# Optimization experiments

Measured on AMD Instinct MI355X. Metric: run time of the kernel, lower is better.

## Reference

```python
import jax, jax.numpy as jnp
import numpy as np

N = 50000   # nodes
C = 128     # in == hidden == out channels (required by residual add)
E = 500000  # edges (before self-loops)
H = 64      # hidden width of pos_nn / attn_nn


def setup_inputs() -> dict:
    key = jax.random.key(0)
    ks = jax.random.split(key, 20)
    s = lambda fan_in: 1.0 / np.sqrt(fan_in)
    d = {}
    d["x"] = jax.random.normal(ks[0], (N, C), jnp.float32)
    d["pos"] = jax.random.uniform(ks[1], (N, 3), jnp.float32)
    d["edge_index"] = jax.random.randint(ks[2], (2, E), 0, N, dtype=jnp.int32)
    # lin_in / lin_out (with bias)
    d["W_in"] = jax.random.normal(ks[3], (C, C), jnp.float32) * s(C)
    d["b_in"] = jnp.zeros((C,), jnp.float32)
    d["W_out"] = jax.random.normal(ks[4], (C, C), jnp.float32) * s(C)
    d["b_out"] = jnp.zeros((C,), jnp.float32)
    # PointTransformerConv internal linears (bias=False in PyG)
    d["W_lin"] = jax.random.normal(ks[5], (C, C), jnp.float32) * s(C)
    d["W_src"] = jax.random.normal(ks[6], (C, C), jnp.float32) * s(C)
    d["W_dst"] = jax.random.normal(ks[7], (C, C), jnp.float32) * s(C)
    # pos_nn: Lin(3,64) -> ReLU -> Lin(64,C)
    d["Wp1"] = jax.random.normal(ks[8], (3, H), jnp.float32) * s(3)
    d["bp1"] = jnp.zeros((H,), jnp.float32)
    d["Wp2"] = jax.random.normal(ks[9], (H, C), jnp.float32) * s(H)
    d["bp2"] = jnp.zeros((C,), jnp.float32)
    # attn_nn: Lin(C,64) -> ReLU -> Lin(64,C)
    d["Wa1"] = jax.random.normal(ks[10], (C, H), jnp.float32) * s(C)
    d["ba1"] = jnp.zeros((H,), jnp.float32)
    d["Wa2"] = jax.random.normal(ks[11], (H, C), jnp.float32) * s(H)
    d["ba2"] = jnp.zeros((C,), jnp.float32)
    return d


def reference(x, pos, edge_index, W_in, b_in, W_out, b_out, W_lin, W_src, W_dst,
              Wp1, bp1, Wp2, bp2, Wa1, ba1, Wa2, ba2):
    n = x.shape[0]
    x_skip = x
    h = jax.nn.relu(x @ W_in + b_in)                      # lin_in + relu, [N,C]
    # PointTransformerConv with add_self_loops=True
    loop = jnp.arange(n, dtype=edge_index.dtype)
    src = jnp.concatenate([edge_index[0], loop])          # j (source)
    dst = jnp.concatenate([edge_index[1], loop])          # i (target)
    a_src = h @ W_src                                      # lin_src(x), [N,C]
    a_dst = h @ W_dst                                      # lin_dst(x), [N,C]
    v = h @ W_lin                                          # lin(x),     [N,C]
    rel = pos[dst] - pos[src]                              # pos_i - pos_j, [Et,3]
    delta = jax.nn.relu(rel @ Wp1 + bp1) @ Wp2 + bp2       # pos_nn, [Et,C]
    alpha = a_dst[dst] - a_src[src] + delta                # alpha_i - alpha_j + delta
    alpha = jax.nn.relu(alpha @ Wa1 + ba1) @ Wa2 + ba2     # attn_nn, [Et,C]
    # per-destination, per-channel softmax over edges
    amax = jax.ops.segment_max(alpha, dst, num_segments=n)
    amax = jnp.where(jnp.isfinite(amax), amax, 0.0)
    ex = jnp.exp(alpha - amax[dst])
    den = jax.ops.segment_sum(ex, dst, num_segments=n) + 1e-16
    w = ex / den[dst]
    out = jax.ops.segment_sum(w * (v[src] + delta), dst, num_segments=n)  # [N,C]
    out = jax.nn.relu(out @ W_out + b_out)                 # lin_out + relu
    return out + x_skip
```

## Files before the change

### kernel.cpp

```cpp
#include <hip/hip_runtime.h>

typedef _Float16 h2_t __attribute__((ext_vector_type(2)));
typedef _Float16 f16x4v __attribute__((ext_vector_type(4)));
typedef _Float16 f16x8 __attribute__((ext_vector_type(8)));
typedef float f32x4 __attribute__((ext_vector_type(4)));

struct F8pair { f16x4v lo, hi; };
static __device__ __forceinline__ f16x8 ldfrag(const _Float16* p) {
    F8pair r;
    r.lo = *(const f16x4v*)p;
    r.hi = *(const f16x4v*)(p + 4);
    return __builtin_bit_cast(f16x8, r);
}

static __device__ __forceinline__ unsigned int pkrtz(float a, float b) {
    return __builtin_bit_cast(unsigned int, __builtin_amdgcn_cvt_pkrtz(a, b));
}

static __device__ __forceinline__ float h2lo(unsigned int w) {
    h2_t h = __builtin_bit_cast(h2_t, w);
    return (float)h.x;
}
static __device__ __forceinline__ float h2hi(unsigned int w) {
    h2_t h = __builtin_bit_cast(h2_t, w);
    return (float)h.y;
}

__global__ void k_pre(const float* __restrict__ W_src, const float* __restrict__ W_dst,
                      const float* __restrict__ Wa1, const float* __restrict__ ba1,
                      const float* __restrict__ Wp2, const float* __restrict__ bp2,
                      const float* __restrict__ Wa2,
                      float* __restrict__ PsW, float* __restrict__ PdW,
                      float* __restrict__ bias2, _Float16* __restrict__ Wcat)
{
    int idx = blockIdx.x * 256 + threadIdx.x;
    if (idx < 8192) {
        int k = idx >> 6, l = idx & 63;
        float a = 0.f;
        for (int c = 0; c < 128; ++c) a = fmaf(W_src[k*128+c], Wa1[c*64+l], a);
        PsW[idx] = a;
    } else if (idx < 16384) {
        int j = idx - 8192; int k = j >> 6, l = j & 63;
        float a = 0.f;
        for (int c = 0; c < 128; ++c) a = fmaf(W_dst[k*128+c], Wa1[c*64+l], a);
        PdW[j] = a;
    } else if (idx < 16448) {
        int l = idx - 16384;
        float a = ba1[l];
        for (int c = 0; c < 128; ++c) a = fmaf(bp2[c], Wa1[c*64+l], a);
        bias2[l] = a;
    } else if (idx < 16448 + 320*68) {
        int j = idx - 16448;
        int row = j / 68, k = j % 68;
        float val = 0.f;
        if (k < 64) {
            if (row < 64) {
                int Q = 2 * (row & 31) + (row >> 5);
                float a = 0.f;
                for (int c = 0; c < 128; ++c) a = fmaf(Wp2[k*128+c], Wa1[c*64+Q], a);
                val = a;
            } else if (row < 192) {
                int cpos = row - 64;
                int P = 2 * (cpos & 63) + (cpos >> 6);
                val = Wp2[k*128 + P];
            } else {
                int cpos = row - 192;
                int P = 2 * (cpos & 63) + (cpos >> 6);
                int Qk = 2 * (k & 31) + (k >> 5);
                val = Wa2[Qk*128 + P];
            }
        }
        Wcat[j] = (_Float16)val;
    }
}

__global__ void k_zero(int* __restrict__ p, int n) {
    int i = blockIdx.x * 256 + threadIdx.x;
    if (i < n) p[i] = 0;
}

__global__ void k_count(const int* __restrict__ ei, int E, int N, int* __restrict__ cnt) {
    int i = blockIdx.x * 256 + threadIdx.x;
    int T = E + N;
    if (i >= T) return;
    int dst = (i < E) ? ei[E + i] : (i - E);
    atomicAdd(&cnt[dst], 1);
}

__global__ void k_pos4(const float* __restrict__ pos, float4* __restrict__ pos4, int N) {
    int i = blockIdx.x * 256 + threadIdx.x;
    if (i < N) pos4[i] = make_float4(pos[3*i], pos[3*i+1], pos[3*i+2], 0.f);
}

__global__ __launch_bounds__(1024) void k_scan1(int* __restrict__ cnt, int* __restrict__ bsum, int N) {
    __shared__ int sc[1024];
    int t = threadIdx.x;
    int i = blockIdx.x * 1024 + t;
    int val = (i < N) ? cnt[i] : 0;
    sc[t] = val;
    __syncthreads();
    for (int off = 1; off < 1024; off <<= 1) {
        int tmp = (t >= off) ? sc[t - off] : 0;
        __syncthreads();
        sc[t] += tmp;
        __syncthreads();
    }
    int incl = sc[t];
    if (i < N) cnt[i] = incl - val;
    if (t == 1023) bsum[blockIdx.x] = incl;
}

__global__ void k_scan2(int* __restrict__ bsum, int* __restrict__ offs, int nb, int N) {
    if (threadIdx.x == 0 && blockIdx.x == 0) {
        int run = 0;
        for (int i = 0; i < nb; ++i) { int tv = bsum[i]; bsum[i] = run; run += tv; }
        offs[N] = run;
    }
}

__global__ void k_scan3(int* __restrict__ offs, const int* __restrict__ bsum,
                        int* __restrict__ cursor, int N) {
    int i = blockIdx.x * 256 + threadIdx.x;
    if (i < N) {
        int o = offs[i] + bsum[i >> 10];
        offs[i] = o;
        cursor[i] = o;
    }
}

__global__ void k_scatter(const int* __restrict__ ei, int E, int N,
                          int* __restrict__ cursor, int* __restrict__ srcs) {
    int i = blockIdx.x * 256 + threadIdx.x;
    int T = E + N;
    if (i >= T) return;
    int s_, d_;
    if (i < E) { s_ = ei[i]; d_ = ei[E + i]; }
    else       { s_ = i - E; d_ = i - E; }
    int p = atomicAdd(&cursor[d_], 1);
    srcs[p] = s_;
}

__global__ __launch_bounds__(256) void k_node(
    const float* __restrict__ x, const float* __restrict__ W_in, const float* __restrict__ b_in,
    const float* __restrict__ W_lin, const float* __restrict__ PsW, const float* __restrict__ PdW,
    const float* __restrict__ bp2,
    unsigned int* __restrict__ vpk, unsigned int* __restrict__ pspk,
    unsigned int* __restrict__ pdpk, int N)
{
    __shared__ float xsT[128][20];
    __shared__ float hsT[128][20];
    int t = threadIdx.x;
    int r0 = blockIdx.x * 16;

    for (int idx = t; idx < 16 * 128; idx += 256) {
        int r = idx >> 7, k = idx & 127;
        int row = r0 + r;
        xsT[k][r] = (row < N) ? x[row * 128 + k] : 0.f;
    }
    __syncthreads();

    int c = t & 127, rg = t >> 7;
    float acc[8];
    {
        float b = b_in[c];
        #pragma unroll
        for (int j = 0; j < 8; ++j) acc[j] = b;
        for (int k = 0; k < 128; ++k) {
            float w = W_in[k * 128 + c];
            const float4 xa = *(const float4*)&xsT[k][rg * 8];
            const float4 xb = *(const float4*)&xsT[k][rg * 8 + 4];
            acc[0] = fmaf(xa.x, w, acc[0]); acc[1] = fmaf(xa.y, w, acc[1]);
            acc[2] = fmaf(xa.z, w, acc[2]); acc[3] = fmaf(xa.w, w, acc[3]);
            acc[4] = fmaf(xb.x, w, acc[4]); acc[5] = fmaf(xb.y, w, acc[5]);
            acc[6] = fmaf(xb.z, w, acc[6]); acc[7] = fmaf(xb.w, w, acc[7]);
        }
        #pragma unroll
        for (int j = 0; j < 8; ++j) hsT[c][rg * 8 + j] = fmaxf(acc[j], 0.f);
    }
    __syncthreads();
    {
        #pragma unroll
        for (int j = 0; j < 8; ++j) acc[j] = 0.f;
        for (int k = 0; k < 128; ++k) {
            float w = W_lin[k * 128 + c];
            const float4 ha = *(const float4*)&hsT[k][rg * 8];
            const float4 hb = *(const float4*)&hsT[k][rg * 8 + 4];
            acc[0] = fmaf(ha.x, w, acc[0]); acc[1] = fmaf(ha.y, w, acc[1]);
            acc[2] = fmaf(ha.z, w, acc[2]); acc[3] = fmaf(ha.w, w, acc[3]);
            acc[4] = fmaf(hb.x, w, acc[4]); acc[5] = fmaf(hb.y, w, acc[5]);
            acc[6] = fmaf(hb.z, w, acc[6]); acc[7] = fmaf(hb.w, w, acc[7]);
        }
        float bpA = bp2[c], bpB = bp2[c | 1];
        #pragma unroll
        for (int j = 0; j < 8; ++j) {
            float partner = __shfl_xor(acc[j], 1);
            int row = r0 + rg * 8 + j;
            if (((c & 1) == 0) && row < N)
                vpk[(size_t)row * 64 + (c >> 1)] = pkrtz(acc[j] + bpA, partner + bpB);
        }
    }
    {
        int c2 = t & 63, g = t >> 6;
        float as[4], ad[4];
        #pragma unroll
        for (int j = 0; j < 4; ++j) { as[j] = 0.f; ad[j] = 0.f; }
        for (int k = 0; k < 128; ++k) {
            float wsv = PsW[k * 64 + c2];
            float wdv = PdW[k * 64 + c2];
            const float4 h4 = *(const float4*)&hsT[k][g * 4];
            as[0] = fmaf(h4.x, wsv, as[0]); as[1] = fmaf(h4.y, wsv, as[1]);
            as[2] = fmaf(h4.z, wsv, as[2]); as[3] = fmaf(h4.w, wsv, as[3]);
            ad[0] = fmaf(h4.x, wdv, ad[0]); ad[1] = fmaf(h4.y, wdv, ad[1]);
            ad[2] = fmaf(h4.z, wdv, ad[2]); ad[3] = fmaf(h4.w, wdv, ad[3]);
        }
        #pragma unroll
        for (int j = 0; j < 4; ++j) {
            float pa = __shfl_xor(as[j], 1);
            float pb = __shfl_xor(ad[j], 1);
            int row = r0 + g * 4 + j;
            if (((c2 & 1) == 0) && row < N) {
                pspk[(size_t)row * 32 + (c2 >> 1)] = pkrtz(as[j], pa);
                pdpk[(size_t)row * 32 + (c2 >> 1)] = pkrtz(ad[j], pb);
            }
        }
    }
}

__global__ __launch_bounds__(512, 2) void k_edge(
    const unsigned int* __restrict__ vpk, const unsigned int* __restrict__ pspk,
    const unsigned int* __restrict__ pdpk,
    const float4* __restrict__ pos4, const int* __restrict__ srcs,
    const int* __restrict__ offs, const _Float16* __restrict__ Wcat,
    const float* __restrict__ Wp1, const float* __restrict__ bp1,
    const float* __restrict__ bias2,
    float* __restrict__ out, int N, int nWavesTot)
{
    __shared__ _Float16 WL[320 * 68];
    __shared__ _Float16 PH[8][16 * 68];
    int tid = threadIdx.x;
    {
        const unsigned int* g = (const unsigned int*)Wcat;
        unsigned int* s = (unsigned int*)WL;
        for (int i = tid; i < 320 * 68 / 2; i += 512) s[i] = g[i];
    }
    __syncthreads();

    int wid = tid >> 6, lane = tid & 63;
    int l15 = lane & 15, akg = lane >> 4;
    _Float16* ph  = PH[wid];
    _Float16* ahv = ph;

    float wp10 = Wp1[lane], wp11 = Wp1[64 + lane], wp12 = Wp1[128 + lane], bp1l = bp1[lane];
    float bias2_r[4];
    #pragma unroll
    for (int nt = 0; nt < 4; ++nt)
        bias2_r[nt] = bias2[2 * ((nt & 1) * 16 + l15) + (nt >> 1)];

    int gw = blockIdx.x * 8 + wid;
    for (int node = gw; node < N; node += nWavesTot) {
        int beg = offs[node], end = offs[node + 1];
        float4 pi = pos4[node];
        unsigned int pdw0 = pdpk[(size_t)node * 32 + l15];
        unsigned int pdw1 = pdpk[(size_t)node * 32 + 16 + l15];
        float base4[4];
        #pragma unroll
        for (int nt = 0; nt < 4; ++nt) {
            unsigned int wd = (nt & 1) ? pdw1 : pdw0;
            base4[nt] = ((nt >> 1) ? h2hi(wd) : h2lo(wd)) + bias2_r[nt];
        }

        float rn[8], rd[8];
        #pragma unroll
        for (int nt = 0; nt < 8; ++nt) { rn[nt] = 0.f; rd[nt] = 0.f; }

        for (int e0 = beg; e0 < end; e0 += 16) {
            int ei_ = e0 + l15;
            int eim = (ei_ < end) ? ei_ : (end - 1);
            int s16 = srcs[eim];
            float4 pj = pos4[s16];
            if (akg == 0) {
                uint2 rr;
                rr.x = pkrtz(pi.x - pj.x, pi.y - pj.y);
                rr.y = pkrtz(pi.z - pj.z, 0.f);
                *(uint2*)&ph[l15 * 68 + 64] = rr;
            }
            #pragma unroll
            for (int ee = 0; ee < 16; ++ee) {
                uint2 rr = *(const uint2*)&ph[ee * 68 + 64];
                float rx = h2lo(rr.x), ry = h2hi(rr.x), rz = h2lo(rr.y);
                float phv = fmaxf(fmaf(rx, wp10, fmaf(ry, wp11, fmaf(rz, wp12, bp1l))), 0.f);
                ph[ee * 68 + lane] = (_Float16)phv;
            }

            f16x8 A0 = ldfrag(&ph[l15 * 68 + akg * 8]);
            f16x8 A1 = ldfrag(&ph[l15 * 68 + 32 + akg * 8]);

            int se[4];
            #pragma unroll
            for (int j = 0; j < 4; ++j) se[j] = __shfl(s16, akg * 4 + j);

            {
                unsigned int psw0[4], psw1[4];
                #pragma unroll
                for (int j = 0; j < 4; ++j) {
                    psw0[j] = pspk[(size_t)se[j] * 32 + l15];
                    psw1[j] = pspk[(size_t)se[j] * 32 + 16 + l15];
                }
                #pragma unroll
                for (int nt = 0; nt < 4; ++nt) {
                    const _Float16* br = &WL[(nt * 16 + l15) * 68];
                    f16x8 B0 = ldfrag(br + akg * 8);
                    f16x8 B1 = ldfrag(br + 32 + akg * 8);
                    f32x4 a = {0.f, 0.f, 0.f, 0.f};
                    a = __builtin_amdgcn_mfma_f32_16x16x32_f16(A0, B0, a, 0, 0, 0);
                    a = __builtin_amdgcn_mfma_f32_16x16x32_f16(A1, B1, a, 0, 0, 0);
                    #pragma unroll
                    for (int j = 0; j < 4; ++j) {
                        unsigned int ws = (nt & 1) ? psw1[j] : psw0[j];
                        float psv = (nt >> 1) ? h2hi(ws) : h2lo(ws);
                        float ahf = fmaxf(a[j] + base4[nt] - psv, 0.f);
                        ahv[(akg * 4 + j) * 68 + nt * 16 + l15] = (_Float16)ahf;
                    }
                }
            }

            f16x8 C0 = ldfrag(&ahv[l15 * 68 + akg * 8]);
            f16x8 C1 = ldfrag(&ahv[l15 * 68 + 32 + akg * 8]);

            #pragma unroll
            for (int hf = 0; hf < 2; ++hf) {
                unsigned int wvA[4], wvB[4];
                #pragma unroll
                for (int j = 0; j < 4; ++j) {
                    wvA[j] = vpk[(size_t)se[j] * 64 + hf * 32 + l15];
                    wvB[j] = vpk[(size_t)se[j] * 64 + hf * 32 + 16 + l15];
                }
                #pragma unroll
                for (int q = 0; q < 4; ++q) {
                    int nt = (q & 1) + hf * 2 + (q >> 1) * 4;
                    const _Float16* br2 = &WL[(64 + nt * 16 + l15) * 68];
                    f16x8 B20 = ldfrag(br2 + akg * 8);
                    f16x8 B21 = ldfrag(br2 + 32 + akg * 8);
                    f32x4 a2 = {0.f, 0.f, 0.f, 0.f};
                    a2 = __builtin_amdgcn_mfma_f32_16x16x32_f16(A0, B20, a2, 0, 0, 0);
                    a2 = __builtin_amdgcn_mfma_f32_16x16x32_f16(A1, B21, a2, 0, 0, 0);
                    const _Float16* br3 = &WL[(192 + nt * 16 + l15) * 68];
                    f16x8 B30 = ldfrag(br3 + akg * 8);
                    f16x8 B31 = ldfrag(br3 + 32 + akg * 8);
                    f32x4 a3 = {0.f, 0.f, 0.f, 0.f};
                    a3 = __builtin_amdgcn_mfma_f32_16x16x32_f16(C0, B30, a3, 0, 0, 0);
                    a3 = __builtin_amdgcn_mfma_f32_16x16x32_f16(C1, B31, a3, 0, 0, 0);
                    #pragma unroll
                    for (int j = 0; j < 4; ++j) {
                        bool vj = (e0 + akg * 4 + j) < end;
                        unsigned int wv = (q & 1) ? wvB[j] : wvA[j];
                        float vv = (q >> 1) ? h2hi(wv) : h2lo(wv);
                        float alpha = vj ? a3[j] : -1e30f;
                        float wexp = __expf(fminf(alpha, 60.f));
                        float u = vv + a2[j];
                        rd[nt] += wexp;
                        rn[nt] = fmaf(wexp, u, rn[nt]);
                    }
                }
            }
        }

        #pragma unroll
        for (int nt = 0; nt < 8; ++nt) {
            rn[nt] += __shfl_xor(rn[nt], 16);
            rn[nt] += __shfl_xor(rn[nt], 32);
            rd[nt] += __shfl_xor(rd[nt], 16);
            rd[nt] += __shfl_xor(rd[nt], 32);
        }
        if (akg == 0) {
            #pragma unroll
            for (int nt2 = 0; nt2 < 4; ++nt2) {
                float2 o;
                o.x = rn[nt2]     / (rd[nt2]     + 1e-16f);
                o.y = rn[nt2 + 4] / (rd[nt2 + 4] + 1e-16f);
                ((float2*)out)[(size_t)node * 64 + nt2 * 16 + l15] = o;
            }
        }
    }
}

__global__ __launch_bounds__(256) void k_out(
    const float* __restrict__ x, const float* __restrict__ W_out, const float* __restrict__ b_out,
    float* __restrict__ out, int N)
{
    __shared__ float csT[128][20];
    int t = threadIdx.x;
    int r0 = blockIdx.x * 16;

    for (int idx = t; idx < 16 * 128; idx += 256) {
        int r = idx >> 7, k = idx & 127;
        int row = r0 + r;
        csT[k][r] = (row < N) ? out[row * 128 + k] : 0.f;
    }
    __syncthreads();

    int c = t & 127, rg = t >> 7;
    float acc[8];
    float b = b_out[c];
    #pragma unroll
    for (int j = 0; j < 8; ++j) acc[j] = b;
    for (int k = 0; k < 128; ++k) {
        float w = W_out[k * 128 + c];
        const float4 ca = *(const float4*)&csT[k][rg * 8];
        const float4 cb = *(const float4*)&csT[k][rg * 8 + 4];
        acc[0] = fmaf(ca.x, w, acc[0]); acc[1] = fmaf(ca.y, w, acc[1]);
        acc[2] = fmaf(ca.z, w, acc[2]); acc[3] = fmaf(ca.w, w, acc[3]);
        acc[4] = fmaf(cb.x, w, acc[4]); acc[5] = fmaf(cb.y, w, acc[5]);
        acc[6] = fmaf(cb.z, w, acc[6]); acc[7] = fmaf(cb.w, w, acc[7]);
    }
    #pragma unroll
    for (int j = 0; j < 8; ++j) {
        int row = r0 + rg * 8 + j;
        if (row < N) out[row * 128 + c] = fmaxf(acc[j], 0.f) + x[row * 128 + c];
    }
}

extern "C" void kernel_launch(void* const* d_in, const int* in_sizes, int n_in,
                              void* d_out, int out_size, void* d_ws, size_t ws_size,
                              hipStream_t stream)
{
    const float* x     = (const float*)d_in[0];
    const float* pos   = (const float*)d_in[1];
    const int*   ei    = (const int*)d_in[2];
    const float* W_in  = (const float*)d_in[3];
    const float* b_in  = (const float*)d_in[4];
    const float* W_out = (const float*)d_in[5];
    const float* b_out = (const float*)d_in[6];
    const float* W_lin = (const float*)d_in[7];
    const float* W_src = (const float*)d_in[8];
    const float* W_dst = (const float*)d_in[9];
    const float* Wp1   = (const float*)d_in[10];
    const float* bp1   = (const float*)d_in[11];
    const float* Wp2   = (const float*)d_in[12];
    const float* bp2   = (const float*)d_in[13];
    const float* Wa1   = (const float*)d_in[14];
    const float* ba1   = (const float*)d_in[15];
    const float* Wa2   = (const float*)d_in[16];
    const float* ba2   = (const float*)d_in[17];
    (void)ba2;

    int N = in_sizes[0] / 128;
    int E = in_sizes[2] / 2;
    int T = E + N;
    float* out = (float*)d_out;

    char* w = (char*)d_ws;
    auto alloc = [&](size_t bytes) -> char* {
        char* p = w;
        w += (bytes + 255) & ~(size_t)255;
        return p;
    };
    unsigned int* vpk  = (unsigned int*)alloc((size_t)N * 64 * 4);
    unsigned int* pspk = (unsigned int*)alloc((size_t)N * 32 * 4);
    unsigned int* pdpk = (unsigned int*)alloc((size_t)N * 32 * 4);
    float4* pos4 = (float4*)alloc((size_t)N * 16);
    float* PsW   = (float*)alloc(8192 * 4);
    float* PdW   = (float*)alloc(8192 * 4);
    float* bias2 = (float*)alloc(64 * 4);
    _Float16* Wcat = (_Float16*)alloc(320 * 68 * 2);
    int*   offs  = (int*)alloc((size_t)(N + 1) * 4);
    int*   cursor= (int*)alloc((size_t)N * 4);
    int*   bsum  = (int*)alloc(256 * 4);
    int*   srcs  = (int*)alloc((size_t)T * 4);

    k_pre<<<dim3((16448 + 320*68 + 255) / 256), dim3(256), 0, stream>>>(
        W_src, W_dst, Wa1, ba1, Wp2, bp2, Wa2, PsW, PdW, bias2, Wcat);
    k_zero<<<dim3((N + 1 + 255) / 256), dim3(256), 0, stream>>>(offs, N + 1);
    k_count<<<dim3((T + 255) / 256), dim3(256), 0, stream>>>(ei, E, N, offs);
    k_pos4<<<dim3((N + 255) / 256), dim3(256), 0, stream>>>(pos, pos4, N);
    int nb = (N + 1023) / 1024;
    k_scan1<<<dim3(nb), dim3(1024), 0, stream>>>(offs, bsum, N);
    k_scan2<<<dim3(1), dim3(64), 0, stream>>>(bsum, offs, nb, N);
    k_scan3<<<dim3((N + 255) / 256), dim3(256), 0, stream>>>(offs, bsum, cursor, N);
    k_scatter<<<dim3((T + 255) / 256), dim3(256), 0, stream>>>(ei, E, N, cursor, srcs);
    k_node<<<dim3((N + 15) / 16), dim3(256), 0, stream>>>(x, W_in, b_in, W_lin, PsW, PdW, bp2,
                                                          vpk, pspk, pdpk, N);
    int nWavesTot = 8192;
    k_edge<<<dim3(1024), dim3(512), 0, stream>>>(vpk, pspk, pdpk, pos4, srcs, offs, Wcat,
                                                 Wp1, bp1, bias2,
                                                 out, N, nWavesTot);
    k_out<<<dim3((N + 15) / 16), dim3(256), 0, stream>>>(x, W_out, b_out, out, N);
}
```

Before: 378.2 us.

## Move node and output dense layers to fp16 MFMA with persistent waves

Replaces the scalar fp32 FMA node kernel (lin_in, lin, and the fused src/dst attention projections) and the output linear kernel with MFMA 16x16x32 fp16 versions. Each kernel is persistent, loads pre-transposed, padded fp16 weights into shared memory once per block, and loops each wave over 16-row tiles. The weight transposition and fp16 conversion move into the precompute kernel. The inputs x and the aggregated features are rounded to fp16, and lin_in's output is also rounded to fp16 between layers, which lowers precision. Each node block now holds about 100KB of shared memory, which limits occupancy.

```diff
diff --git a/kernel.cpp b/kernel.cpp
--- a/kernel.cpp
+++ b/kernel.cpp
@@ -26,31 +26,31 @@
     return (float)h.y;
 }
 
+static __device__ __forceinline__ f16x8 mkfrag(const float* p) {
+    float4 a = ((const float4*)p)[0];
+    float4 b = ((const float4*)p)[1];
+    uint4 u;
+    u.x = pkrtz(a.x, a.y); u.y = pkrtz(a.z, a.w);
+    u.z = pkrtz(b.x, b.y); u.w = pkrtz(b.z, b.w);
+    return __builtin_bit_cast(f16x8, u);
+}
+
 __global__ void k_pre(const float* __restrict__ W_src, const float* __restrict__ W_dst,
                       const float* __restrict__ Wa1, const float* __restrict__ ba1,
                       const float* __restrict__ Wp2, const float* __restrict__ bp2,
-                      const float* __restrict__ Wa2,
-                      float* __restrict__ PsW, float* __restrict__ PdW,
-                      float* __restrict__ bias2, _Float16* __restrict__ Wcat)
+                      const float* __restrict__ Wa2, const float* __restrict__ W_in,
+                      const float* __restrict__ W_lin, const float* __restrict__ W_out,
+                      float* __restrict__ bias2, _Float16* __restrict__ Wcat,
+                      _Float16* __restrict__ Wnode, _Float16* __restrict__ WoutT)
 {
     int idx = blockIdx.x * 256 + threadIdx.x;
-    if (idx < 8192) {
-        int k = idx >> 6, l = idx & 63;
-        float a = 0.f;
-        for (int c = 0; c < 128; ++c) a = fmaf(W_src[k*128+c], Wa1[c*64+l], a);
-        PsW[idx] = a;
-    } else if (idx < 16384) {
-        int j = idx - 8192; int k = j >> 6, l = j & 63;
-        float a = 0.f;
-        for (int c = 0; c < 128; ++c) a = fmaf(W_dst[k*128+c], Wa1[c*64+l], a);
-        PdW[j] = a;
-    } else if (idx < 16448) {
-        int l = idx - 16384;
+    if (idx < 64) {
+        int l = idx;
         float a = ba1[l];
         for (int c = 0; c < 128; ++c) a = fmaf(bp2[c], Wa1[c*64+l], a);
         bias2[l] = a;
-    } else if (idx < 16448 + 320*68) {
-        int j = idx - 16448;
+    } else if (idx < 64 + 21760) {
+        int j = idx - 64;
         int row = j / 68, k = j % 68;
         float val = 0.f;
         if (k < 64) {
@@ -71,6 +71,30 @@
             }
         }
         Wcat[j] = (_Float16)val;
+    } else if (idx < 21824 + 16896) {
+        int j = idx - 21824;
+        int c = j / 132, k = j % 132;
+        Wnode[j] = (_Float16)((k < 128) ? W_in[k*128+c] : 0.f);
+    } else if (idx < 38720 + 16896) {
+        int j = idx - 38720;
+        int c = j / 132, k = j % 132;
+        Wnode[16896 + j] = (_Float16)((k < 128) ? W_lin[k*128+c] : 0.f);
+    } else if (idx < 55616 + 16896) {
+        int j = idx - 55616;
+        int c = j / 132, k = j % 132;
+        float val = 0.f;
+        if (k < 128) {
+            if (c < 64) {
+                for (int q = 0; q < 128; ++q) val = fmaf(W_src[k*128+q], Wa1[q*64+c], val);
+            } else {
+                for (int q = 0; q < 128; ++q) val = fmaf(W_dst[k*128+q], Wa1[q*64+(c-64)], val);
+            }
+        }
+        Wnode[33792 + j] = (_Float16)val;
+    } else if (idx < 72512 + 16896) {
+        int j = idx - 72512;
+        int c = j / 132, k = j % 132;
+        WoutT[j] = (_Float16)((k < 128) ? W_out[k*128+c] : 0.f);
     }
 }
 
@@ -140,87 +164,90 @@
     srcs[p] = s_;
 }
 
-__global__ __launch_bounds__(256) void k_node(
-    const float* __restrict__ x, const float* __restrict__ W_in, const float* __restrict__ b_in,
-    const float* __restrict__ W_lin, const float* __restrict__ PsW, const float* __restrict__ PdW,
-    const float* __restrict__ bp2,
+__global__ __launch_bounds__(512) void k_node2(
+    const float* __restrict__ x, const float* __restrict__ b_in,
+    const float* __restrict__ bp2, const _Float16* __restrict__ Wnode,
     unsigned int* __restrict__ vpk, unsigned int* __restrict__ pspk,
-    unsigned int* __restrict__ pdpk, int N)
+    unsigned int* __restrict__ pdpk, int N, int nTiles, int nWavesTot)
 {
-    __shared__ float xsT[128][20];
-    __shared__ float hsT[128][20];
-    int t = threadIdx.x;
-    int r0 = blockIdx.x * 16;
-
-    for (int idx = t; idx < 16 * 128; idx += 256) {
-        int r = idx >> 7, k = idx & 127;
-        int row = r0 + r;
-        xsT[k][r] = (row < N) ? x[row * 128 + k] : 0.f;
+    __shared__ _Float16 WB[3 * 16896];
+    __shared__ _Float16 HT[8][16 * 132];
+    int tid = threadIdx.x;
+    {
+        const unsigned int* g = (const unsigned int*)Wnode;
+        unsigned int* s = (unsigned int*)WB;
+        for (int i = tid; i < 3 * 16896 / 2; i += 512) s[i] = g[i];
     }
     __syncthreads();
 
-    int c = t & 127, rg = t >> 7;
-    float acc[8];
-    {
-        float b = b_in[c];
-        #pragma unroll
-        for (int j = 0; j < 8; ++j) acc[j] = b;
-        for (int k = 0; k < 128; ++k) {
-            float w = W_in[k * 128 + c];
-            const float4 xa = *(const float4*)&xsT[k][rg * 8];
-            const float4 xb = *(const float4*)&xsT[k][rg * 8 + 4];
-            acc[0] = fmaf(xa.x, w, acc[0]); acc[1] = fmaf(xa.y, w, acc[1]);
-            acc[2] = fmaf(xa.z, w, acc[2]); acc[3] = fmaf(xa.w, w, acc[3]);
-            acc[4] = fmaf(xb.x, w, acc[4]); acc[5] = fmaf(xb.y, w, acc[5]);
-            acc[6] = fmaf(xb.z, w, acc[6]); acc[7] = fmaf(xb.w, w, acc[7]);
-        }
-        #pragma unroll
-        for (int j = 0; j < 8; ++j) hsT[c][rg * 8 + j] = fmaxf(acc[j], 0.f);
-    }
-    __syncthreads();
-    {
-        #pragma unroll
-        for (int j = 0; j < 8; ++j) acc[j] = 0.f;
-        for (int k = 0; k < 128; ++k) {
-            float w = W_lin[k * 128 + c];
-            const float4 ha = *(const float4*)&hsT[k][rg * 8];
-            const float4 hb = *(const float4*)&hsT[k][rg * 8 + 4];
-            acc[0] = fmaf(ha.x, w, acc[0]); acc[1] = fmaf(ha.y, w, acc[1]);
-            acc[2] = fmaf(ha.z, w, acc[2]); acc[3] = fmaf(ha.w, w, acc[3]);
-            acc[4] = fmaf(hb.x, w, acc[4]); acc[5] = fmaf(hb.y, w, acc[5]);
-            acc[6] = fmaf(hb.z, w, acc[6]); acc[7] = fmaf(hb.w, w, acc[7]);
-        }
-        float bpA = bp2[c], bpB = bp2[c | 1];
-        #pragma unroll
-        for (int j = 0; j < 8; ++j) {
-            float partner = __shfl_xor(acc[j], 1);
-            int row = r0 + rg * 8 + j;
-            if (((c & 1) == 0) && row < N)
-                vpk[(size_t)row * 64 + (c >> 1)] = pkrtz(acc[j] + bpA, partner + bpB);
-        }
-    }
-    {
-        int c2 = t & 63, g = t >> 6;
-        float as[4], ad[4];
-        #pragma unroll
-        for (int j = 0; j < 4; ++j) { as[j] = 0.f; ad[j] = 0.f; }
-        for (int k = 0; k < 128; ++k) {
-            float wsv = PsW[k * 64 + c2];
-            float wdv = PdW[k * 64 + c2];
-            const float4 h4 = *(const float4*)&hsT[k][g * 4];
-            as[0] = fmaf(h4.x, wsv, as[0]); as[1] = fmaf(h4.y, wsv, as[1]);
-            as[2] = fmaf(h4.z, wsv, as[2]); as[3] = fmaf(h4.w, wsv, as[3]);
-            ad[0] = fmaf(h4.x, wdv, ad[0]); ad[1] = fmaf(h4.y, wdv, ad[1]);
-            ad[2] = fmaf(h4.z, wdv, ad[2]); ad[3] = fmaf(h4.w, wdv, ad[3]);
-        }
-        #pragma unroll
-        for (int j = 0; j < 4; ++j) {
-            float pa = __shfl_xor(as[j], 1);
-            float pb = __shfl_xor(ad[j], 1);
-            int row = r0 + g * 4 + j;
-            if (((c2 & 1) == 0) && row < N) {
-                pspk[(size_t)row * 32 + (c2 >> 1)] = pkrtz(as[j], pa);
-                pdpk[(size_t)row * 32 + (c2 >> 1)] = pkrtz(ad[j], pb);
+    int wid = tid >> 6, lane = tid & 63;
+    int l15 = lane & 15, akg = lane >> 4;
+    _Float16* ht = HT[wid];
+
+    int gw = blockIdx.x * 8 + wid;
+    for (int t = gw; t < nTiles; t += nWavesTot) {
+        int row0 = t * 16;
+        int rowa = row0 + l15; if (rowa > N - 1) rowa = N - 1;
+
+        f16x8 A[4];
+        #pragma unroll
+        for (int f = 0; f < 4; ++f)
+            A[f] = mkfrag(&x[(size_t)rowa * 128 + f * 32 + akg * 8]);
+
+        #pragma unroll
+        for (int ct = 0; ct < 8; ++ct) {
+            const _Float16* bb = &WB[(ct * 16 + l15) * 132];
+            f32x4 d = {0.f, 0.f, 0.f, 0.f};
+            #pragma unroll
+            for (int f = 0; f < 4; ++f)
+                d = __builtin_amdgcn_mfma_f32_16x16x32_f16(A[f], ldfrag(bb + f * 32 + akg * 8), d, 0, 0, 0);
+            float bin = b_in[ct * 16 + l15];
+            #pragma unroll
+            for (int j = 0; j < 4; ++j)
+                ht[(akg * 4 + j) * 132 + ct * 16 + l15] = (_Float16)fmaxf(d[j] + bin, 0.f);
+        }
+
+        f16x8 H[4];
+        #pragma unroll
+        for (int f = 0; f < 4; ++f)
+            H[f] = ldfrag(&ht[l15 * 132 + f * 32 + akg * 8]);
+
+        #pragma unroll
+        for (int ct = 0; ct < 8; ++ct) {
+            const _Float16* bb = &WB[16896 + (ct * 16 + l15) * 132];
+            f32x4 d = {0.f, 0.f, 0.f, 0.f};
+            #pragma unroll
+            for (int f = 0; f < 4; ++f)
+                d = __builtin_amdgcn_mfma_f32_16x16x32_f16(H[f], ldfrag(bb + f * 32 + akg * 8), d, 0, 0, 0);
+            float bp = bp2[ct * 16 + l15];
+            #pragma unroll
+            for (int j = 0; j < 4; ++j) {
+                float val = d[j] + bp;
+                float partner = __shfl_xor(val, 1);
+                int row = row0 + akg * 4 + j;
+                if (((l15 & 1) == 0) && row < N)
+                    vpk[(size_t)row * 64 + ct * 8 + (l15 >> 1)] = pkrtz(val, partner);
+            }
+        }
+
+        #pragma unroll
+        for (int ct = 0; ct < 8; ++ct) {
+            const _Float16* bb = &WB[33792 + (ct * 16 + l15) * 132];
+            f32x4 d = {0.f, 0.f, 0.f, 0.f};
+            #pragma unroll
+            for (int f = 0; f < 4; ++f)
+                d = __builtin_amdgcn_mfma_f32_16x16x32_f16(H[f], ldfrag(bb + f * 32 + akg * 8), d, 0, 0, 0);
+            #pragma unroll
+            for (int j = 0; j < 4; ++j) {
+                float val = d[j];
+                float partner = __shfl_xor(val, 1);
+                int row = row0 + akg * 4 + j;
+                if (((l15 & 1) == 0) && row < N) {
+                    if (ct < 4)
+                        pspk[(size_t)row * 32 + ct * 8 + (l15 >> 1)] = pkrtz(val, partner);
+                    else
+                        pdpk[(size_t)row * 32 + (ct - 4) * 8 + (l15 >> 1)] = pkrtz(val, partner);
+                }
             }
         }
     }
@@ -384,39 +411,50 @@
     }
 }
 
-__global__ __launch_bounds__(256) void k_out(
-    const float* __restrict__ x, const float* __restrict__ W_out, const float* __restrict__ b_out,
-    float* __restrict__ out, int N)
+__global__ __launch_bounds__(256) void k_out2(
+    const float* __restrict__ x, const float* __restrict__ b_out,
+    const _Float16* __restrict__ WoutT, float* __restrict__ out,
+    int N, int nTiles, int nWavesTot)
 {
-    __shared__ float csT[128][20];
-    int t = threadIdx.x;
-    int r0 = blockIdx.x * 16;
-
-    for (int idx = t; idx < 16 * 128; idx += 256) {
-        int r = idx >> 7, k = idx & 127;
-        int row = r0 + r;
-        csT[k][r] = (row < N) ? out[row * 128 + k] : 0.f;
+    __shared__ _Float16 WB[16896];
+    int tid = threadIdx.x;
+    {
+        const unsigned int* g = (const unsigned int*)WoutT;
+        unsigned int* s = (unsigned int*)WB;
+        for (int i = tid; i < 16896 / 2; i += 256) s[i] = g[i];
     }
     __syncthreads();
 
-    int c = t & 127, rg = t >> 7;
-    float acc[8];
-    float b = b_out[c];
-    #pragma unroll
-    for (int j = 0; j < 8; ++j) acc[j] = b;
-    for (int k = 0; k < 128; ++k) {
-        float w = W_out[k * 128 + c];
-        const float4 ca = *(const float4*)&csT[k][rg * 8];
-        const float4 cb = *(const float4*)&csT[k][rg * 8 + 4];
-        acc[0] = fmaf(ca.x, w, acc[0]); acc[1] = fmaf(ca.y, w, acc[1]);
-        acc[2] = fmaf(ca.z, w, acc[2]); acc[3] = fmaf(ca.w, w, acc[3]);
-        acc[4] = fmaf(cb.x, w, acc[4]); acc[5] = fmaf(cb.y, w, acc[5]);
-        acc[6] = fmaf(cb.z, w, acc[6]); acc[7] = fmaf(cb.w, w, acc[7]);
-    }
-    #pragma unroll
-    for (int j = 0; j < 8; ++j) {
-        int row = r0 + rg * 8 + j;
-        if (row < N) out[row * 128 + c] = fmaxf(acc[j], 0.f) + x[row * 128 + c];
+    int wid = tid >> 6, lane = tid & 63;
+    int l15 = lane & 15, akg = lane >> 4;
+
+    int gw = blockIdx.x * 4 + wid;
+    for (int t = gw; t < nTiles; t += nWavesTot) {
+        int row0 = t * 16;
+        int rowa = row0 + l15; if (rowa > N - 1) rowa = N - 1;
+
+        f16x8 A[4];
+        #pragma unroll
+        for (int f = 0; f < 4; ++f)
+            A[f] = mkfrag(&out[(size_t)rowa * 128 + f * 32 + akg * 8]);
+
+        #pragma unroll
+        for (int ct = 0; ct < 8; ++ct) {
+            const _Float16* bb = &WB[(ct * 16 + l15) * 132];
+            f32x4 d = {0.f, 0.f, 0.f, 0.f};
+            #pragma unroll
+            for (int f = 0; f < 4; ++f)
+                d = __builtin_amdgcn_mfma_f32_16x16x32_f16(A[f], ldfrag(bb + f * 32 + akg * 8), d, 0, 0, 0);
+            float bo = b_out[ct * 16 + l15];
+            #pragma unroll
+            for (int j = 0; j < 4; ++j) {
+                int row = row0 + akg * 4 + j;
+                if (row < N) {
+                    int c = ct * 16 + l15;
+                    out[(size_t)row * 128 + c] = fmaxf(d[j] + bo, 0.f) + x[(size_t)row * 128 + c];
+                }
+            }
+        }
     }
 }
 
@@ -447,6 +485,7 @@
     int N = in_sizes[0] / 128;
     int E = in_sizes[2] / 2;
     int T = E + N;
+    int nTiles = (N + 15) / 16;
     float* out = (float*)d_out;
 
     char* w = (char*)d_ws;
@@ -459,17 +498,18 @@
     unsigned int* pspk = (unsigned int*)alloc((size_t)N * 32 * 4);
     unsigned int* pdpk = (unsigned int*)alloc((size_t)N * 32 * 4);
     float4* pos4 = (float4*)alloc((size_t)N * 16);
-    float* PsW   = (float*)alloc(8192 * 4);
-    float* PdW   = (float*)alloc(8192 * 4);
     float* bias2 = (float*)alloc(64 * 4);
-    _Float16* Wcat = (_Float16*)alloc(320 * 68 * 2);
+    _Float16* Wcat  = (_Float16*)alloc(21760 * 2);
+    _Float16* Wnode = (_Float16*)alloc(3 * 16896 * 2);
+    _Float16* WoutT = (_Float16*)alloc(16896 * 2);
     int*   offs  = (int*)alloc((size_t)(N + 1) * 4);
     int*   cursor= (int*)alloc((size_t)N * 4);
     int*   bsum  = (int*)alloc(256 * 4);
     int*   srcs  = (int*)alloc((size_t)T * 4);
 
-    k_pre<<<dim3((16448 + 320*68 + 255) / 256), dim3(256), 0, stream>>>(
-        W_src, W_dst, Wa1, ba1, Wp2, bp2, Wa2, PsW, PdW, bias2, Wcat);
+    k_pre<<<dim3((89408 + 255) / 256), dim3(256), 0, stream>>>(
+        W_src, W_dst, Wa1, ba1, Wp2, bp2, Wa2, W_in, W_lin, W_out,
+        bias2, Wcat, Wnode, WoutT);
     k_zero<<<dim3((N + 1 + 255) / 256), dim3(256), 0, stream>>>(offs, N + 1);
     k_count<<<dim3((T + 255) / 256), dim3(256), 0, stream>>>(ei, E, N, offs);
     k_pos4<<<dim3((N + 255) / 256), dim3(256), 0, stream>>>(pos, pos4, N);
@@ -478,11 +518,16 @@
     k_scan2<<<dim3(1), dim3(64), 0, stream>>>(bsum, offs, nb, N);
     k_scan3<<<dim3((N + 255) / 256), dim3(256), 0, stream>>>(offs, bsum, cursor, N);
     k_scatter<<<dim3((T + 255) / 256), dim3(256), 0, stream>>>(ei, E, N, cursor, srcs);
-    k_node<<<dim3((N + 15) / 16), dim3(256), 0, stream>>>(x, W_in, b_in, W_lin, PsW, PdW, bp2,
-                                                          vpk, pspk, pdpk, N);
+
+    int nodeBlocks = 192;
+    k_node2<<<dim3(nodeBlocks), dim3(512), 0, stream>>>(x, b_in, bp2, Wnode,
+                                                        vpk, pspk, pdpk, N, nTiles,
+                                                        nodeBlocks * 8);
     int nWavesTot = 8192;
     k_edge<<<dim3(1024), dim3(512), 0, stream>>>(vpk, pspk, pdpk, pos4, srcs, offs, Wcat,
                                                  Wp1, bp1, bias2,
                                                  out, N, nWavesTot);
-    k_out<<<dim3((N + 15) / 16), dim3(256), 0, stream>>>(x, W_out, b_out, out, N);
-}
+    int outBlocks = 256;
+    k_out2<<<dim3(outBlocks), dim3(256), 0, stream>>>(x, b_out, WoutT, out, N, nTiles,
+                                                      outBlocks * 4);
+}
```

After: 334.6 us. 11.5% less time.
